# Kernel optimization log

Measured on AMD Instinct MI355X. Metric: run time of the kernel, lower is better.

## Reference

```python
import jax, jax.numpy as jnp
import numpy as np

B, S, K_IN = 8, 2048, 512
D_MODEL, N_INPUT, N_PROCESS = 1024, 4096, 2048
K = 256


def setup_inputs() -> dict:
    key = jax.random.key(0)
    k1, k2, k3, k4 = jax.random.split(key, 4)
    return {
        "selected_activations": jax.random.normal(k1, (B, S, K_IN), dtype=jnp.float32),
        "selected_indices": jax.random.randint(k2, (B, K_IN), 0, N_INPUT, dtype=jnp.int64),
        "k": K,
        "combination_weights": jax.random.normal(k3, (N_PROCESS, N_INPUT), dtype=jnp.float32),
        "output_projections": jax.random.normal(k4, (N_PROCESS, D_MODEL), dtype=jnp.float32),
    }


def reference(selected_activations, selected_indices, k, combination_weights, output_projections):
    # Gather per-batch combination weights: [n_process, B, k_in] -> [B, n_process, k_in]
    sel_w = jnp.take(combination_weights, selected_indices, axis=1)  # [P, B, k_in]
    sel_w = jnp.transpose(sel_w, (1, 0, 2))                          # [B, P, k_in]
    # Batched matmul + exact GELU (torch F.gelu default is erf-based)
    process_act = jax.nn.gelu(
        jnp.einsum("bsk,bpk->bsp", selected_activations, sel_w), approximate=False
    )  # [B, S, P]
    # Top-k gating over mean activation across sequence
    process_scores = process_act.mean(axis=1)                        # [B, P]
    _, proc_idx = jax.lax.top_k(process_scores, k)                   # [B, k]
    # Gather selected process activations along last dim
    sel_proc_act = jnp.take_along_axis(process_act, proc_idx[:, None, :], axis=2)  # [B, S, k]
    # Gather output projections per batch: [B, k, d_model]
    sel_proj = output_projections[proc_idx]                          # [B, k, D]
    return jnp.einsum("bsk,bkd->bsd", sel_proc_act, sel_proj)        # [B, S, D]
```

## Files before the change

kernel.cpp:

```cpp
#include <hip/hip_runtime.h>
#include <hip/hip_bf16.h>
#include <math.h>

#define B_    8
#define S_    2048
#define KIN_  512
#define NIN_  4096
#define P_    2048
#define D_    1024
#define KSEL_ 256

typedef __attribute__((ext_vector_type(8))) short short8;
typedef __attribute__((ext_vector_type(4))) float f32x4;

__device__ __forceinline__ unsigned short f2bf(float f) {
    unsigned u = __float_as_uint(f);
    unsigned r = (u + 0x7fffu + ((u >> 16) & 1u)) >> 16;
    return (unsigned short)r;
}
__device__ __forceinline__ float bf2f(unsigned short h) {
    return __uint_as_float(((unsigned)h) << 16);
}
__device__ __forceinline__ float gelu_exact(float x) {
    return 0.5f * x * (1.0f + erff(x * 0.70710678118654752f));
}
__device__ __forceinline__ void gl2lds16(const void* g, void* l) {
    __builtin_amdgcn_global_load_lds(
        (const __attribute__((address_space(1))) unsigned int*)g,
        (__attribute__((address_space(3))) unsigned int*)l, 16, 0, 0);
}


__global__ __launch_bounds__(256) void prep_kernel(
        const float* __restrict__ A, const float* __restrict__ W,
        const int* __restrict__ idx,
        unsigned short* __restrict__ Ahi, unsigned short* __restrict__ AloF,
        unsigned short* __restrict__ Ghi, unsigned short* __restrict__ Glo) {
    __shared__ float wrow_s[NIN_];
    __shared__ int   ibs8[B_ * KIN_];
    int id = blockIdx.x;
    int t  = threadIdx.x;
    if (id < 1024) {
        int b = id >> 7, rb = id & 127;
        int l = t & 63, wv = t >> 6;
        int lr = l & 15, quad = l >> 4;
        const float* src = A + ((size_t)(b * S_ + rb * 16 + lr)) * KIN_ + quad * 8;
        unsigned short* dh = Ahi + ((size_t)(b * S_ + rb * 16 + lr)) * KIN_ + quad * 8;
        unsigned short* dl = AloF + (size_t)b * 1048576 + (size_t)rb * 512 + (size_t)l * 8;
        for (int kb = wv; kb < 16; kb += 4) {
            float4 v0 = *(const float4*)(src + kb * 32);
            float4 v1 = *(const float4*)(src + kb * 32 + 4);
            float vv[8] = {v0.x, v0.y, v0.z, v0.w, v1.x, v1.y, v1.z, v1.w};
            short8 h8, l8;
#pragma unroll
            for (int jj = 0; jj < 8; jj++) {
                unsigned short h = f2bf(vv[jj]);
                h8[jj] = (short)h;
                l8[jj] = (short)f2bf(vv[jj] - bf2f(h));
            }
            *(short8*)(dh + kb * 32) = h8;
            *(short8*)(dl + (size_t)kb * 65536) = l8;
        }
    } else {
        int p = id - 1024;
        const float* wrow = W + (size_t)p * NIN_;
#pragma unroll
        for (int i = 0; i < 4; i++)
            *(float4*)(wrow_s + (t + i * 256) * 4) =
                *(const float4*)(wrow + (t + i * 256) * 4);
#pragma unroll
        for (int i = 0; i < 16; i++)
            ibs8[t + i * 256] = idx[t + i * 256];
        __syncthreads();
        int wv = t >> 6, tt = t & 63;
#pragma unroll
        for (int bi = 0; bi < 2; ++bi) {
            int b = wv * 2 + bi;
            size_t o = ((size_t)b * P_ + p) * KIN_;
            const int* ib = ibs8 + b * KIN_;
            short8 h8, l8;
#pragma unroll
            for (int e = 0; e < 8; e++) {
                float v = wrow_s[ib[tt * 8 + e]];
                unsigned short h = f2bf(v);
                h8[e] = (short)h;
                l8[e] = (short)f2bf(v - bf2f(h));
            }
            *(short8*)(Ghi + o + tt * 8) = h8;
            *(short8*)(Glo + o + tt * 8) = l8;
        }
    }
}

template <bool STORE_C>
__global__ __launch_bounds__(256, 3) void gemm1_score(
        const unsigned short* __restrict__ Ahi, const unsigned short* __restrict__ AloF,
        const unsigned short* __restrict__ Ghi, const unsigned short* __restrict__ Glo,
        float* __restrict__ scores, unsigned short* __restrict__ C) {
    __shared__ __align__(16) unsigned short lds[24576];

    int d    = blockIdx.x;
    int xcd  = d & 7;
    int slot = d >> 3;
    int c    = (slot >> 4) * 8 + xcd;
    int j    = slot & 15;
    int b    = c >> 4;
    int rc   = c & 15;
    int p0   = ((rc & 3) * 4 + (j & 3)) * 128;
    int s0   = ((rc >> 2) * 4 + (j >> 2)) * 128;

    const int t  = threadIdx.x;
    const int w = t >> 6, l = t & 63;
    const int wm = w & 1, wn = w >> 1;
    const int lr = l & 15, quad = l >> 4;

    const int srow = t >> 2;
    const int koff = ((t & 3) ^ ((t >> 3) & 3)) * 8;
    const size_t baseA = ((size_t)(b * S_ + s0)) * KIN_;
    const size_t baseG = ((size_t)(b * P_ + p0)) * KIN_;
    const unsigned short* pA0 = Ahi + baseA + (size_t)srow * KIN_ + koff;
    const unsigned short* pA1 = pA0 + (size_t)64 * KIN_;
    const unsigned short* pG0 = Ghi + baseG + (size_t)srow * KIN_ + koff;
    const unsigned short* pG1 = pG0 + (size_t)64 * KIN_;
    const unsigned short* pH0 = Glo + baseG + (size_t)srow * KIN_ + koff;
    const unsigned short* pH1 = pH0 + (size_t)64 * KIN_;
    const unsigned short* alB = AloF + (size_t)b * 1048576
                              + (size_t)((s0 >> 4) + wm * 4) * 512 + (size_t)l * 8;
    char* lb = (char*)lds + w * 1024;

    int ra[4], rg[4];
#pragma unroll
    for (int i = 0; i < 4; i++) {
        int rowa = wm * 64 + i * 16 + lr;
        int rowg = wn * 64 + i * 16 + lr;
        ra[i] = rowa * 32 + (quad ^ ((rowa >> 1) & 3)) * 8;
        rg[i] = rowg * 32 + (quad ^ ((rowg >> 1) & 3)) * 8;
    }

    f32x4 acc[4][4];
#pragma unroll
    for (int i = 0; i < 4; i++)
#pragma unroll
        for (int jj = 0; jj < 4; jj++) acc[i][jj] = (f32x4){0.f, 0.f, 0.f, 0.f};

    auto issue = [&](int k0, int buf) {
        char* dst = lb + buf * 24576;
        gl2lds16(pA0 + k0, dst + 0);
        gl2lds16(pA1 + k0, dst + 4096);
        gl2lds16(pG0 + k0, dst + 8192);
        gl2lds16(pG1 + k0, dst + 12288);
        gl2lds16(pH0 + k0, dst + 16384);
        gl2lds16(pH1 + k0, dst + 20480);
    };

    issue(0, 0);
    for (int it = 0; it < KIN_ / 32; ++it) {
        short8 alc[4];
#pragma unroll
        for (int mt = 0; mt < 4; mt++)
            alc[mt] = *(const short8*)(alB + (size_t)it * 65536 + mt * 512);
        if (it + 1 < KIN_ / 32) {
            issue((it + 1) * 32, (it + 1) & 1);
            asm volatile("s_waitcnt vmcnt(10)\n\ts_barrier" ::: "memory");
        } else {
            asm volatile("s_waitcnt vmcnt(0)\n\ts_barrier" ::: "memory");
        }
        const unsigned short* Lb = lds + (it & 1) * 12288;

        short8 gh[4], gl8[4];
#pragma unroll
        for (int i = 0; i < 4; i++) {
            gh[i]  = *(const short8*)(Lb + 4096 + rg[i]);
            gl8[i] = *(const short8*)(Lb + 8192 + rg[i]);
        }
#pragma unroll
        for (int mt = 0; mt < 4; mt++) {
            short8 ah = *(const short8*)(Lb + ra[mt]);
#pragma unroll
            for (int nt = 0; nt < 4; nt++) {
                acc[mt][nt] = __builtin_amdgcn_mfma_f32_16x16x32_bf16(ah,      gh[nt],  acc[mt][nt], 0, 0, 0);
                acc[mt][nt] = __builtin_amdgcn_mfma_f32_16x16x32_bf16(ah,      gl8[nt], acc[mt][nt], 0, 0, 0);
                acc[mt][nt] = __builtin_amdgcn_mfma_f32_16x16x32_bf16(alc[mt], gh[nt],  acc[mt][nt], 0, 0, 0);
            }
        }
        asm volatile("s_barrier" ::: "memory");
    }

    float colsum[4] = {0.f, 0.f, 0.f, 0.f};
#pragma unroll
    for (int mt = 0; mt < 4; mt++)
#pragma unroll
        for (int nt = 0; nt < 4; nt++)
#pragma unroll
            for (int r = 0; r < 4; r++) {
                float g = gelu_exact(acc[mt][nt][r]);
                colsum[nt] += g;
                acc[mt][nt][r] = g;
            }
#pragma unroll
    for (int nt = 0; nt < 4; nt++) {
        colsum[nt] += __shfl_xor(colsum[nt], 16);
        colsum[nt] += __shfl_xor(colsum[nt], 32);
    }
    if (quad == 0) {
#pragma unroll
        for (int nt = 0; nt < 4; nt++)
            atomicAdd(&scores[b * P_ + p0 + wn * 64 + nt * 16 + lr], colsum[nt]);
    }

    if (STORE_C) {
#pragma unroll
        for (int mt = 0; mt < 4; mt++)
#pragma unroll
            for (int nt = 0; nt < 4; nt++)
#pragma unroll
                for (int r = 0; r < 4; r++) {
                    int row = wm * 64 + mt * 16 + quad * 4 + r;
                    int col = wn * 64 + nt * 16 + lr;
                    lds[row * 136 + col] = f2bf(acc[mt][nt][r]);
                }
        __syncthreads();
        for (int i = t; i < 2048; i += 256) {
            int row = i >> 4, ch = i & 15;
            uint4 v = *(const uint4*)(lds + row * 136 + ch * 8);
            *(uint4*)(C + ((size_t)(b * S_ + s0 + row)) * P_ + p0 + ch * 8) = v;
        }
    }
}

__global__ __launch_bounds__(1024) void topk_kernel(const float* __restrict__ scores,
                                                    int* __restrict__ pidx) {
    __shared__ float v[2048];
    __shared__ int   ix[2048];
    int b = blockIdx.x;
    int t = threadIdx.x;
    for (int i = t; i < 2048; i += 1024) { v[i] = scores[b * 2048 + i]; ix[i] = i; }
    __syncthreads();
    for (int k = 2; k <= 2048; k <<= 1) {
        for (int j = k >> 1; j > 0; j >>= 1) {
            for (int i = t; i < 2048; i += 1024) {
                int o = i ^ j;
                if (o > i) {
                    bool desc = ((i & k) == 0);
                    float va = v[i], vb = v[o];
                    int ia = ix[i], ib = ix[o];
                    bool b_first = (vb > va) || (vb == va && ib < ia);
                    if (desc == b_first) { v[i] = vb; v[o] = va; ix[i] = ib; ix[o] = ia; }
                }
            }
            __syncthreads();
        }
    }
    for (int k = 2; k <= 256; k <<= 1) {
        for (int j = k >> 1; j > 0; j >>= 1) {
            if (t < 256) {
                int i = t, o = i ^ j;
                if (o > i) {
                    bool asc = ((i & k) == 0);
                    int a = ix[i], c2 = ix[o];
                    if ((a > c2) == asc) { ix[i] = c2; ix[o] = a; }
                }
            }
            __syncthreads();
        }
    }
    if (t < KSEL_) pidx[b * KSEL_ + t] = ix[t];
}

__global__ __launch_bounds__(256) void gathers_kernel(
        const unsigned short* __restrict__ C, const float* __restrict__ proj,
        const int* __restrict__ pidx,
        unsigned short* __restrict__ selact, unsigned short* __restrict__ PselT,
        int base) {
    __shared__ int pj[256];
    __shared__ unsigned short tile[64][65];
    int id = blockIdx.x + base, t = threadIdx.x;
    if (id < 2048) {
        int b = id >> 8;
        pj[t] = pidx[b * KSEL_ + t];
        __syncthreads();
        size_t r0 = (size_t)b * S_ + (id & 255) * 8;
#pragma unroll
        for (int r = 0; r < 8; ++r) {
            size_t row = r0 + r;
            selact[row * KSEL_ + t] = C[row * P_ + pj[t]];
        }
    } else {
        int g = id - 2048;
        int d0 = (g & 15) * 64, k0 = ((g >> 4) & 3) * 64, b = g >> 6;
        int tr = t >> 6;
        int tc = t & 63;
#pragma unroll
        for (int r = 0; r < 16; r++) {
            int kk = r * 4 + tr;
            int prow = pidx[b * KSEL_ + k0 + kk];
            tile[kk][tc] = f2bf(proj[(size_t)prow * D_ + d0 + tc]);
        }
        __syncthreads();
#pragma unroll
        for (int r = 0; r < 16; r++) {
            int dd = r * 4 + tr;
            PselT[((size_t)(b * D_ + d0 + dd)) * KSEL_ + k0 + tc] = tile[tc][dd];
        }
    }
}

__global__ __launch_bounds__(256) void gemm1b_selact(
        const unsigned short* __restrict__ Ahi, const unsigned short* __restrict__ AloF,
        const unsigned short* __restrict__ Ghi, const unsigned short* __restrict__ Glo,
        const int* __restrict__ pidx, unsigned short* __restrict__ selact) {
    __shared__ __align__(16) unsigned short lds[16384];

    const int t  = threadIdx.x;
    const int b  = blockIdx.z;
    const int s0 = blockIdx.y * 128;
    const int n0 = blockIdx.x * 128;
    const int w = t >> 6, l = t & 63;
    const int wm = w & 1, wn = w >> 1;
    const int lr = l & 15, quad = l >> 4;

    const int srow = t >> 2;
    const int koff = ((t & 3) ^ ((t >> 3) & 3)) * 8;
    const size_t baseA = ((size_t)(b * S_ + s0)) * KIN_;
    const size_t offA0 = baseA + (size_t)srow * KIN_ + koff;
    const size_t offA1 = offA0 + (size_t)64 * KIN_;
    const int prow0 = pidx[b * KSEL_ + n0 + srow];
    const int prow1 = pidx[b * KSEL_ + n0 + 64 + srow];
    const size_t offG0 = ((size_t)(b * P_ + prow0)) * KIN_ + koff;
    const size_t offG1 = ((size_t)(b * P_ + prow1)) * KIN_ + koff;
    const unsigned short* alB = AloF + (size_t)b * 1048576
                              + (size_t)((s0 >> 4) + wm * 4) * 512 + (size_t)l * 8;
    char* lb = (char*)lds + w * 1024;

    int ra[4], rg[4];
#pragma unroll
    for (int i = 0; i < 4; i++) {
        int rowa = wm * 64 + i * 16 + lr;
        int rowg = wn * 64 + i * 16 + lr;
        ra[i] = rowa * 32 + (quad ^ ((rowa >> 1) & 3)) * 8;
        rg[i] = rowg * 32 + (quad ^ ((rowg >> 1) & 3)) * 8;
    }

    f32x4 acc[4][4];
#pragma unroll
    for (int i = 0; i < 4; i++)
#pragma unroll
        for (int jj = 0; jj < 4; jj++) acc[i][jj] = (f32x4){0.f, 0.f, 0.f, 0.f};

    for (int k0 = 0; k0 < KIN_; k0 += 32) {
        int kb = k0 >> 5;
        gl2lds16(Ahi + offA0 + k0, lb + 0);
        gl2lds16(Ahi + offA1 + k0, lb + 4096);
        gl2lds16(Ghi + offG0 + k0, lb + 8192);
        gl2lds16(Ghi + offG1 + k0, lb + 12288);
        gl2lds16(Glo + offG0 + k0, lb + 16384);
        gl2lds16(Glo + offG1 + k0, lb + 20480);
        short8 alc[4];
#pragma unroll
        for (int i = 0; i < 4; i++)
            alc[i] = *(const short8*)(alB + (size_t)kb * 65536 + i * 512);
        __syncthreads();

        short8 gh[4], gl8[4];
#pragma unroll
        for (int i = 0; i < 4; i++) {
            gh[i]  = *(const short8*)(lds + 4096 + rg[i]);
            gl8[i] = *(const short8*)(lds + 8192 + rg[i]);
        }
#pragma unroll
        for (int mt = 0; mt < 4; mt++) {
            short8 ah = *(const short8*)(lds + ra[mt]);
#pragma unroll
            for (int nt = 0; nt < 4; nt++) {
                acc[mt][nt] = __builtin_amdgcn_mfma_f32_16x16x32_bf16(ah,      gh[nt],  acc[mt][nt], 0, 0, 0);
                acc[mt][nt] = __builtin_amdgcn_mfma_f32_16x16x32_bf16(ah,      gl8[nt], acc[mt][nt], 0, 0, 0);
                acc[mt][nt] = __builtin_amdgcn_mfma_f32_16x16x32_bf16(alc[mt], gh[nt],  acc[mt][nt], 0, 0, 0);
            }
        }
        __syncthreads();
    }

#pragma unroll
    for (int mt = 0; mt < 4; mt++)
#pragma unroll
        for (int nt = 0; nt < 4; nt++)
#pragma unroll
            for (int r = 0; r < 4; r++) {
                int row = wm * 64 + mt * 16 + quad * 4 + r;
                int col = wn * 64 + nt * 16 + lr;
                lds[row * 128 + col] = f2bf(gelu_exact(acc[mt][nt][r]));
            }
    __syncthreads();
    for (int i = t; i < 2048; i += 256) {
        int row = i >> 4, ch = i & 15;
        uint4 v = *(const uint4*)(lds + row * 128 + ch * 8);
        *(uint4*)(selact + ((size_t)(b * S_ + s0 + row)) * KSEL_ + n0 + ch * 8) = v;
    }
}

__global__ __launch_bounds__(256) void gemm2_mfma(
        const unsigned short* __restrict__ selact,
        const unsigned short* __restrict__ PselT,
        float* __restrict__ out) {
    __shared__ __align__(16) unsigned short lds[16384];

    const int t  = threadIdx.x;
    const int b  = blockIdx.z;
    const int s0 = blockIdx.y * 128;
    const int d0 = blockIdx.x * 128;
    const int w = t >> 6, l = t & 63;
    const int wm = w & 1, wn = w >> 1;
    const int lr = l & 15, quad = l >> 4;

    const int srow = t >> 2;
    const int koff = ((t & 3) ^ ((t >> 3) & 3)) * 8;
    const unsigned short* pA0 = selact + ((size_t)(b * S_ + s0 + srow)) * KSEL_ + koff;
    const unsigned short* pA1 = pA0 + (size_t)64 * KSEL_;
    const unsigned short* pB0 = PselT + ((size_t)(b * D_ + d0 + srow)) * KSEL_ + koff;
    const unsigned short* pB1 = pB0 + (size_t)64 * KSEL_;
    char* lb = (char*)lds + w * 1024;

    int ra[4], rg[4];
#pragma unroll
    for (int i = 0; i < 4; i++) {
        int rowa = wm * 64 + i * 16 + lr;
        int rowg = wn * 64 + i * 16 + lr;
        ra[i] = rowa * 32 + (quad ^ ((rowa >> 1) & 3)) * 8;
        rg[i] = rowg * 32 + (quad ^ ((rowg >> 1) & 3)) * 8;
    }

    f32x4 acc[4][4];
#pragma unroll
    for (int i = 0; i < 4; i++)
#pragma unroll
        for (int jj = 0; jj < 4; jj++) acc[i][jj] = (f32x4){0.f, 0.f, 0.f, 0.f};

    auto issue = [&](int k0, int buf) {
        char* dst = lb + buf * 16384;
        gl2lds16(pA0 + k0, dst + 0);
        gl2lds16(pA1 + k0, dst + 4096);
        gl2lds16(pB0 + k0, dst + 8192);
        gl2lds16(pB1 + k0, dst + 12288);
    };

    issue(0, 0);
    for (int it = 0; it < KSEL_ / 32; ++it) {
        if (it + 1 < KSEL_ / 32) {
            issue((it + 1) * 32, (it + 1) & 1);
            asm volatile("s_waitcnt vmcnt(4)\n\ts_barrier" ::: "memory");
        } else {
            asm volatile("s_waitcnt vmcnt(0)\n\ts_barrier" ::: "memory");
        }
        const unsigned short* Lb = lds + (it & 1) * 8192;

        short8 af[4], bf[4];
#pragma unroll
        for (int i = 0; i < 4; i++) {
            af[i] = *(const short8*)(Lb + ra[i]);
            bf[i] = *(const short8*)(Lb + 4096 + rg[i]);
        }
#pragma unroll
        for (int mt = 0; mt < 4; mt++)
#pragma unroll
            for (int nt = 0; nt < 4; nt++)
                acc[mt][nt] = __builtin_amdgcn_mfma_f32_16x16x32_bf16(af[mt], bf[nt], acc[mt][nt], 0, 0, 0);
        asm volatile("s_barrier" ::: "memory");
    }

#pragma unroll
    for (int mt = 0; mt < 4; mt++)
#pragma unroll
        for (int nt = 0; nt < 4; nt++)
#pragma unroll
            for (int r = 0; r < 4; r++)
                out[((size_t)(b * S_ + s0 + wm * 64 + mt * 16 + quad * 4 + r)) * D_
                    + d0 + wn * 64 + nt * 16 + lr] = acc[mt][nt][r];
}

extern "C" void kernel_launch(void* const* d_in, const int* in_sizes, int n_in,
                              void* d_out, int out_size, void* d_ws, size_t ws_size,
                              hipStream_t stream) {
    (void)in_sizes; (void)n_in; (void)out_size;
    const float* act  = (const float*)d_in[0];
    const int*   idx  = (const int*)d_in[1];
    const float* W    = (const float*)d_in[3];
    const float* proj = (const float*)d_in[4];
    float*       out  = (float*)d_out;

    char* ws = (char*)d_ws;
    unsigned short* Ahi    = (unsigned short*)(ws + 0);
    unsigned short* AloF   = (unsigned short*)(ws + 16777216);
    unsigned short* Ghi    = (unsigned short*)(ws + 33554432);
    unsigned short* Glo    = (unsigned short*)(ws + 50331648);
    float*          scores = (float*)(ws + 67108864);
    int*            pidx   = (int*)(ws + 67174400);
    unsigned short* selact = (unsigned short*)(ws + 67182592);
    unsigned short* PselT  = (unsigned short*)(ws + 75571200);
    unsigned short* Cbf    = (unsigned short*)(ws + 79765504);
    const bool big = ws_size >= 146874368ull;

    hipMemsetAsync(scores, 0, B_ * P_ * sizeof(float), stream);

    prep_kernel<<<dim3(1024 + P_), 256, 0, stream>>>(act, W, idx, Ahi, AloF, Ghi, Glo);

    if (big) {
        gemm1_score<true><<<dim3(2048), 256, 0, stream>>>(Ahi, AloF, Ghi, Glo, scores, Cbf);
        topk_kernel<<<dim3(B_), 1024, 0, stream>>>(scores, pidx);
        gathers_kernel<<<dim3(2048 + 512), 256, 0, stream>>>(Cbf, proj, pidx, selact, PselT, 0);
    } else {
        gemm1_score<false><<<dim3(2048), 256, 0, stream>>>(Ahi, AloF, Ghi, Glo, scores, nullptr);
        topk_kernel<<<dim3(B_), 1024, 0, stream>>>(scores, pidx);
        gemm1b_selact<<<dim3(KSEL_ / 128, S_ / 128, B_), 256, 0, stream>>>(
            Ahi, AloF, Ghi, Glo, pidx, selact);
        gathers_kernel<<<dim3(512), 256, 0, stream>>>(Cbf, proj, pidx, selact, PselT, 2048);
    }
    gemm2_mfma<<<dim3(D_ / 128, S_ / 128, B_), 256, 0, stream>>>(selact, PselT, out);
}
```

Measured before the change: 355.6 us.

## Enlarge gemm1 tiles to 256x256 with 8 waves and staged loads

Switches the first GEMM from 128x128 tiles with 4 waves to 256x256 tiles with 8 waves (512 threads, 512 blocks), so each staged A and G tile feeds more MFMAs and global plus LDS traffic per FLOP drops. The K-loop is split into four sub-phases that interleave the A, G-hi and G-lo async loads with MFMA groups, with the low-part activation loads prefetched in registers. MFMA sections are wrapped in s_setprio. In exchange it uses more LDS and more accumulator registers per thread, allows fewer resident blocks (launch bounds 512,2), adds more barriers, and stores the C tile in two halves.

```diff
diff --git a/kernel.cpp b/kernel.cpp
--- a/kernel.cpp
+++ b/kernel.cpp
@@ -92,26 +92,40 @@
     }
 }
 
+#define MFMA16(m0, A0, A1, AL0, AL1)                                                                      \
+    _Pragma("unroll")                                                                                     \
+    for (int nt = 0; nt < 4; nt++) {                                                                      \
+        acc[m0][nt]     = __builtin_amdgcn_mfma_f32_16x16x32_bf16(A0, gh[nt], acc[m0][nt], 0, 0, 0);      \
+        acc[m0][nt]     = __builtin_amdgcn_mfma_f32_16x16x32_bf16(A0, gl[nt], acc[m0][nt], 0, 0, 0);      \
+        acc[m0 + 1][nt] = __builtin_amdgcn_mfma_f32_16x16x32_bf16(A1, gh[nt], acc[m0 + 1][nt], 0, 0, 0);  \
+        acc[m0 + 1][nt] = __builtin_amdgcn_mfma_f32_16x16x32_bf16(A1, gl[nt], acc[m0 + 1][nt], 0, 0, 0);  \
+    }                                                                                                     \
+    _Pragma("unroll")                                                                                     \
+    for (int nt = 0; nt < 4; nt++) {                                                                      \
+        acc[m0][nt]     = __builtin_amdgcn_mfma_f32_16x16x32_bf16(AL0, gh[nt], acc[m0][nt], 0, 0, 0);     \
+        acc[m0 + 1][nt] = __builtin_amdgcn_mfma_f32_16x16x32_bf16(AL1, gh[nt], acc[m0 + 1][nt], 0, 0, 0); \
+    }
+
 template <bool STORE_C>
-__global__ __launch_bounds__(256, 3) void gemm1_score(
+__global__ __launch_bounds__(512, 2) void gemm1_score(
         const unsigned short* __restrict__ Ahi, const unsigned short* __restrict__ AloF,
         const unsigned short* __restrict__ Ghi, const unsigned short* __restrict__ Glo,
         float* __restrict__ scores, unsigned short* __restrict__ C) {
-    __shared__ __align__(16) unsigned short lds[24576];
+    __shared__ __align__(16) unsigned short lds[49152];
 
     int d    = blockIdx.x;
     int xcd  = d & 7;
-    int slot = d >> 3;
-    int c    = (slot >> 4) * 8 + xcd;
-    int j    = slot & 15;
-    int b    = c >> 4;
-    int rc   = c & 15;
-    int p0   = ((rc & 3) * 4 + (j & 3)) * 128;
-    int s0   = ((rc >> 2) * 4 + (j >> 2)) * 128;
-
-    const int t  = threadIdx.x;
+    int s2   = d >> 3;
+    int cid  = (s2 >> 2) * 8 + xcd;
+    int j    = s2 & 3;
+    int b    = cid >> 4;
+    int rc   = cid & 15;
+    int p0   = ((rc & 3) * 2 + (j & 1)) * 256;
+    int s0   = ((rc >> 2) * 2 + (j >> 1)) * 256;
+
+    const int t = threadIdx.x;
     const int w = t >> 6, l = t & 63;
-    const int wm = w & 1, wn = w >> 1;
+    const int wm = w >> 2, wn = w & 3;
     const int lr = l & 15, quad = l >> 4;
 
     const int srow = t >> 2;
@@ -119,76 +133,132 @@
     const size_t baseA = ((size_t)(b * S_ + s0)) * KIN_;
     const size_t baseG = ((size_t)(b * P_ + p0)) * KIN_;
     const unsigned short* pA0 = Ahi + baseA + (size_t)srow * KIN_ + koff;
-    const unsigned short* pA1 = pA0 + (size_t)64 * KIN_;
+    const unsigned short* pA1 = pA0 + (size_t)128 * KIN_;
     const unsigned short* pG0 = Ghi + baseG + (size_t)srow * KIN_ + koff;
-    const unsigned short* pG1 = pG0 + (size_t)64 * KIN_;
+    const unsigned short* pG1 = pG0 + (size_t)128 * KIN_;
     const unsigned short* pH0 = Glo + baseG + (size_t)srow * KIN_ + koff;
-    const unsigned short* pH1 = pH0 + (size_t)64 * KIN_;
+    const unsigned short* pH1 = pH0 + (size_t)128 * KIN_;
     const unsigned short* alB = AloF + (size_t)b * 1048576
-                              + (size_t)((s0 >> 4) + wm * 4) * 512 + (size_t)l * 8;
+                              + (size_t)((s0 >> 4) + wm * 8) * 512 + (size_t)l * 8;
     char* lb = (char*)lds + w * 1024;
 
-    int ra[4], rg[4];
+    int ra[8], rg[4];
+#pragma unroll
+    for (int i = 0; i < 8; i++) {
+        int row = wm * 128 + i * 16 + lr;
+        ra[i] = row * 32 + (quad ^ ((row >> 1) & 3)) * 8;
+    }
 #pragma unroll
     for (int i = 0; i < 4; i++) {
-        int rowa = wm * 64 + i * 16 + lr;
-        int rowg = wn * 64 + i * 16 + lr;
-        ra[i] = rowa * 32 + (quad ^ ((rowa >> 1) & 3)) * 8;
-        rg[i] = rowg * 32 + (quad ^ ((rowg >> 1) & 3)) * 8;
-    }
-
-    f32x4 acc[4][4];
-#pragma unroll
-    for (int i = 0; i < 4; i++)
+        int row = wn * 64 + i * 16 + lr;
+        rg[i] = row * 32 + (quad ^ ((row >> 1) & 3)) * 8;
+    }
+
+    f32x4 acc[8][4];
+#pragma unroll
+    for (int i = 0; i < 8; i++)
 #pragma unroll
         for (int jj = 0; jj < 4; jj++) acc[i][jj] = (f32x4){0.f, 0.f, 0.f, 0.f};
 
-    auto issue = [&](int k0, int buf) {
-        char* dst = lb + buf * 24576;
+    auto issueA = [&](int k0, int bf) {
+        char* dst = lb + bf * 49152;
         gl2lds16(pA0 + k0, dst + 0);
-        gl2lds16(pA1 + k0, dst + 4096);
-        gl2lds16(pG0 + k0, dst + 8192);
-        gl2lds16(pG1 + k0, dst + 12288);
-        gl2lds16(pH0 + k0, dst + 16384);
-        gl2lds16(pH1 + k0, dst + 20480);
+        gl2lds16(pA1 + k0, dst + 8192);
     };
-
-    issue(0, 0);
-    for (int it = 0; it < KIN_ / 32; ++it) {
-        short8 alc[4];
-#pragma unroll
-        for (int mt = 0; mt < 4; mt++)
-            alc[mt] = *(const short8*)(alB + (size_t)it * 65536 + mt * 512);
-        if (it + 1 < KIN_ / 32) {
-            issue((it + 1) * 32, (it + 1) & 1);
-            asm volatile("s_waitcnt vmcnt(10)\n\ts_barrier" ::: "memory");
+    auto issueG = [&](int k0, int bf) {
+        char* dst = lb + bf * 49152;
+        gl2lds16(pG0 + k0, dst + 16384);
+        gl2lds16(pG1 + k0, dst + 24576);
+    };
+    auto issueH = [&](int k0, int bf) {
+        char* dst = lb + bf * 49152;
+        gl2lds16(pH0 + k0, dst + 32768);
+        gl2lds16(pH1 + k0, dst + 40960);
+    };
+
+    issueA(0, 0); issueG(0, 0); issueH(0, 0);
+    short8 alc0 = *(const short8*)(alB);
+    short8 alc1 = *(const short8*)(alB + 512);
+    short8 gh[4], gl[4];
+
+    for (int it = 0; it < 16; ++it) {
+        const unsigned short* Lb = lds + (it & 1) * 24576;
+        const unsigned short* aB = alB + (size_t)it * 65536;
+        const int nk  = (it + 1) * 32;
+        const int nbf = (it + 1) & 1;
+        const bool more = it < 15;
+        short8 aln0, aln1;
+
+        aln0 = *(const short8*)(aB + 1024);
+        aln1 = *(const short8*)(aB + 1536);
+        if (more) {
+            issueA(nk, nbf);
+            asm volatile("s_waitcnt vmcnt(4)\n\ts_barrier" ::: "memory");
         } else {
-            asm volatile("s_waitcnt vmcnt(0)\n\ts_barrier" ::: "memory");
-        }
-        const unsigned short* Lb = lds + (it & 1) * 12288;
-
-        short8 gh[4], gl8[4];
-#pragma unroll
-        for (int i = 0; i < 4; i++) {
-            gh[i]  = *(const short8*)(Lb + 4096 + rg[i]);
-            gl8[i] = *(const short8*)(Lb + 8192 + rg[i]);
-        }
-#pragma unroll
-        for (int mt = 0; mt < 4; mt++) {
-            short8 ah = *(const short8*)(Lb + ra[mt]);
-#pragma unroll
-            for (int nt = 0; nt < 4; nt++) {
-                acc[mt][nt] = __builtin_amdgcn_mfma_f32_16x16x32_bf16(ah,      gh[nt],  acc[mt][nt], 0, 0, 0);
-                acc[mt][nt] = __builtin_amdgcn_mfma_f32_16x16x32_bf16(ah,      gl8[nt], acc[mt][nt], 0, 0, 0);
-                acc[mt][nt] = __builtin_amdgcn_mfma_f32_16x16x32_bf16(alc[mt], gh[nt],  acc[mt][nt], 0, 0, 0);
-            }
-        }
-        asm volatile("s_barrier" ::: "memory");
+            asm volatile("s_waitcnt vmcnt(2)\n\ts_barrier" ::: "memory");
+        }
+        {
+#pragma unroll
+            for (int i = 0; i < 4; i++) {
+                gh[i] = *(const short8*)(Lb + 8192 + rg[i]);
+                gl[i] = *(const short8*)(Lb + 16384 + rg[i]);
+            }
+            short8 a0 = *(const short8*)(Lb + ra[0]);
+            short8 a1 = *(const short8*)(Lb + ra[1]);
+            __builtin_amdgcn_s_setprio(1);
+            MFMA16(0, a0, a1, alc0, alc1)
+            __builtin_amdgcn_s_setprio(0);
+            asm volatile("s_barrier" ::: "memory");
+        }
+        alc0 = aln0; alc1 = aln1;
+
+        aln0 = *(const short8*)(aB + 2048);
+        aln1 = *(const short8*)(aB + 2560);
+        {
+            short8 a0 = *(const short8*)(Lb + ra[2]);
+            short8 a1 = *(const short8*)(Lb + ra[3]);
+            if (more) issueG(nk, nbf);
+            asm volatile("s_barrier" ::: "memory");
+            __builtin_amdgcn_s_setprio(1);
+            MFMA16(2, a0, a1, alc0, alc1)
+            __builtin_amdgcn_s_setprio(0);
+            asm volatile("s_barrier" ::: "memory");
+        }
+        alc0 = aln0; alc1 = aln1;
+
+        aln0 = *(const short8*)(aB + 3072);
+        aln1 = *(const short8*)(aB + 3584);
+        {
+            short8 a0 = *(const short8*)(Lb + ra[4]);
+            short8 a1 = *(const short8*)(Lb + ra[5]);
+            if (more) issueH(nk, nbf);
+            asm volatile("s_barrier" ::: "memory");
+            __builtin_amdgcn_s_setprio(1);
+            MFMA16(4, a0, a1, alc0, alc1)
+            __builtin_amdgcn_s_setprio(0);
+            asm volatile("s_barrier" ::: "memory");
+        }
+        alc0 = aln0; alc1 = aln1;
+
+        if (more) {
+            aln0 = *(const short8*)(aB + 65536);
+            aln1 = *(const short8*)(aB + 65536 + 512);
+        }
+        {
+            short8 a0 = *(const short8*)(Lb + ra[6]);
+            short8 a1 = *(const short8*)(Lb + ra[7]);
+            asm volatile("s_barrier" ::: "memory");
+            __builtin_amdgcn_s_setprio(1);
+            MFMA16(6, a0, a1, alc0, alc1)
+            __builtin_amdgcn_s_setprio(0);
+            asm volatile("s_barrier" ::: "memory");
+        }
+        if (more) { alc0 = aln0; alc1 = aln1; }
     }
 
     float colsum[4] = {0.f, 0.f, 0.f, 0.f};
 #pragma unroll
-    for (int mt = 0; mt < 4; mt++)
+    for (int mt = 0; mt < 8; mt++)
 #pragma unroll
         for (int nt = 0; nt < 4; nt++)
 #pragma unroll
@@ -210,20 +280,26 @@
 
     if (STORE_C) {
 #pragma unroll
-        for (int mt = 0; mt < 4; mt++)
-#pragma unroll
-            for (int nt = 0; nt < 4; nt++)
-#pragma unroll
-                for (int r = 0; r < 4; r++) {
-                    int row = wm * 64 + mt * 16 + quad * 4 + r;
-                    int col = wn * 64 + nt * 16 + lr;
-                    lds[row * 136 + col] = f2bf(acc[mt][nt][r]);
-                }
-        __syncthreads();
-        for (int i = t; i < 2048; i += 256) {
-            int row = i >> 4, ch = i & 15;
-            uint4 v = *(const uint4*)(lds + row * 136 + ch * 8);
-            *(uint4*)(C + ((size_t)(b * S_ + s0 + row)) * P_ + p0 + ch * 8) = v;
+        for (int h = 0; h < 2; h++) {
+            __syncthreads();
+            if (wm == h) {
+#pragma unroll
+                for (int mt = 0; mt < 8; mt++)
+#pragma unroll
+                    for (int nt = 0; nt < 4; nt++)
+#pragma unroll
+                        for (int r = 0; r < 4; r++) {
+                            int row = mt * 16 + quad * 4 + r;
+                            int col = wn * 64 + nt * 16 + lr;
+                            lds[row * 256 + col] = f2bf(acc[mt][nt][r]);
+                        }
+            }
+            __syncthreads();
+            for (int i = t; i < 4096; i += 512) {
+                int row = i >> 5, ch = i & 31;
+                uint4 v = *(const uint4*)(lds + row * 256 + ch * 8);
+                *(uint4*)(C + ((size_t)(b * S_ + s0 + h * 128 + row)) * P_ + p0 + ch * 8) = v;
+            }
         }
     }
 }
@@ -504,11 +580,11 @@
     prep_kernel<<<dim3(1024 + P_), 256, 0, stream>>>(act, W, idx, Ahi, AloF, Ghi, Glo);
 
     if (big) {
-        gemm1_score<true><<<dim3(2048), 256, 0, stream>>>(Ahi, AloF, Ghi, Glo, scores, Cbf);
+        gemm1_score<true><<<dim3(512), 512, 0, stream>>>(Ahi, AloF, Ghi, Glo, scores, Cbf);
         topk_kernel<<<dim3(B_), 1024, 0, stream>>>(scores, pidx);
         gathers_kernel<<<dim3(2048 + 512), 256, 0, stream>>>(Cbf, proj, pidx, selact, PselT, 0);
     } else {
-        gemm1_score<false><<<dim3(2048), 256, 0, stream>>>(Ahi, AloF, Ghi, Glo, scores, nullptr);
+        gemm1_score<false><<<dim3(512), 512, 0, stream>>>(Ahi, AloF, Ghi, Glo, scores, nullptr);
         topk_kernel<<<dim3(B_), 1024, 0, stream>>>(scores, pidx);
         gemm1b_selact<<<dim3(KSEL_ / 128, S_ / 128, B_), 256, 0, stream>>>(
             Ahi, AloF, Ghi, Glo, pidx, selact);
```

Result: slower. 413.6 us (+16.3%).
